# Optimization experiments

Measured on AMD Instinct MI355X. Metric: run time of the kernel, lower is better.

Reference implementation:

```python
import jax, jax.numpy as jnp
import numpy as np

EMBED_DIM = 2048
NUM_HEADS = 16
NUM_KV_GROUPS = 4
HEAD_DIM = EMBED_DIM // NUM_HEADS  # 128


def setup_inputs() -> dict:
    key = jax.random.key(0)
    ks = jax.random.split(key, 9)
    B, S, E = 2, 2048, EMBED_DIM
    kv_dim = HEAD_DIM * NUM_KV_GROUPS
    sc = 1.0 / np.sqrt(E)
    return {
        "x": jax.random.normal(ks[0], (B, S, E), dtype=jnp.float32),
        "Wq": jax.random.normal(ks[1], (E, E), dtype=jnp.float32) * sc,
        "bq": jnp.zeros((E,), dtype=jnp.float32),
        "Wk": jax.random.normal(ks[2], (E, kv_dim), dtype=jnp.float32) * sc,
        "bk": jnp.zeros((kv_dim,), dtype=jnp.float32),
        "Wv": jax.random.normal(ks[3], (E, kv_dim), dtype=jnp.float32) * sc,
        "bv": jnp.zeros((kv_dim,), dtype=jnp.float32),
        "Wo": jax.random.normal(ks[4], (E, E), dtype=jnp.float32) * sc,
        "bo": jnp.zeros((E,), dtype=jnp.float32),
    }


def reference(x, Wq, bq, Wk, bk, Wv, bv, Wo, bo):
    B, S, E = x.shape
    H, G, D = NUM_HEADS, NUM_KV_GROUPS, HEAD_DIM
    R = H // G  # heads per kv group
    # projections
    Q = (x @ Wq + bq).reshape(B, S, H, D).transpose(0, 2, 1, 3)   # [B,H,S,D]
    K = (x @ Wk + bk).reshape(B, S, G, D).transpose(0, 2, 1, 3)   # [B,G,S,D]
    V = (x @ Wv + bv).reshape(B, S, G, D).transpose(0, 2, 1, 3)   # [B,G,S,D]
    # GQA: broadcast KV groups over head subgroups instead of repeat_interleave copy
    Qg = Q.reshape(B, G, R, S, D)
    scores = jnp.einsum('bgrsd,bgtd->bgrst', Qg, K) / np.sqrt(D)  # [B,G,R,S,S]
    weights = jax.nn.softmax(scores, axis=-1)
    out = jnp.einsum('bgrst,bgtd->bgrsd', weights, V)             # [B,G,R,S,D]
    out = out.reshape(B, H, S, D).transpose(0, 2, 1, 3).reshape(B, S, E)
    return out @ Wo + bo
```

## Files before the change

kernel.cpp:

```cpp
#include <hip/hip_runtime.h>
#include <hip/hip_bf16.h>


typedef __attribute__((ext_vector_type(8))) short bf16x8;
typedef __attribute__((ext_vector_type(4))) short bf16x4;
typedef __attribute__((ext_vector_type(4))) float f32x4;

#define MFMA_16x16x32(a, b, c) __builtin_amdgcn_mfma_f32_16x16x32_bf16((a), (b), (c), 0, 0, 0)

__device__ __forceinline__ unsigned short f2bf(float x) {
  union { float f; unsigned int u; } c;
  c.f = x;
  unsigned int u = c.u;
  return (unsigned short)((u + 0x7fffu + ((u >> 16) & 1u)) >> 16);
}

__device__ __forceinline__ unsigned short f2bf_hw(float x) {
  __hip_bfloat16 h = __float2bfloat16(x);
  union { __hip_bfloat16 h; unsigned short u; } c;
  c.h = h;
  return c.u;
}

__device__ __forceinline__ void gload_lds16(const void* g, void* l) {
  __builtin_amdgcn_global_load_lds(
      (const __attribute__((address_space(1))) unsigned int*)g,
      (__attribute__((address_space(3))) unsigned int*)l, 16, 0, 0);
}

__global__ void cast_x_kernel(const float* __restrict__ x,
                              unsigned short* __restrict__ out, long n) {
  long i = ((long)blockIdx.x * blockDim.x + threadIdx.x) * 8;
  if (i >= n) return;
  float4 a = *reinterpret_cast<const float4*>(x + i);
  float4 b = *reinterpret_cast<const float4*>(x + i + 4);
  union { unsigned short s[8]; bf16x8 v; } o;
  o.s[0] = f2bf(a.x); o.s[1] = f2bf(a.y); o.s[2] = f2bf(a.z); o.s[3] = f2bf(a.w);
  o.s[4] = f2bf(b.x); o.s[5] = f2bf(b.y); o.s[6] = f2bf(b.z); o.s[7] = f2bf(b.w);
  *reinterpret_cast<bf16x8*>(out + i) = o.v;
}

__global__ void prep_w_kernel(const float* __restrict__ Wq,
                              const float* __restrict__ Wk,
                              const float* __restrict__ Wv,
                              const float* __restrict__ Wo,
                              unsigned short* __restrict__ WqkvT,
                              unsigned short* __restrict__ WoT) {
  __shared__ float t[32][33];
  const int tx = threadIdx.x, ty = threadIdx.y;
  const int ng = blockIdx.x * 32;
  const int k0 = blockIdx.y * 32;
  const float* src;
  int srcN, n0;
  unsigned short* dst;
  if (ng < 2048)      { src = Wq; srcN = 2048; n0 = ng;        dst = WqkvT + (size_t)ng * 2048; }
  else if (ng < 2560) { src = Wk; srcN = 512;  n0 = ng - 2048; dst = WqkvT + (size_t)ng * 2048; }
  else if (ng < 3072) { src = Wv; srcN = 512;  n0 = ng - 2560; dst = WqkvT + (size_t)ng * 2048; }
  else                { src = Wo; srcN = 2048; n0 = ng - 3072; dst = WoT + (size_t)(ng - 3072) * 2048; }
#pragma unroll
  for (int i = 0; i < 4; i++)
    t[ty + i * 8][tx] = src[(size_t)(k0 + ty + i * 8) * srcN + n0 + tx];
  __syncthreads();
#pragma unroll
  for (int i = 0; i < 4; i++)
    dst[(size_t)(ty + i * 8) * 2048 + k0 + tx] = f2bf(t[tx][ty + i * 8]);
}

__global__ void concat_bias_kernel(const float* __restrict__ bq,
                                   const float* __restrict__ bk,
                                   const float* __restrict__ bv,
                                   float* __restrict__ out) {
  int i = blockIdx.x * 256 + threadIdx.x;
  if (i >= 3072) return;
  out[i] = (i < 2048) ? bq[i] : (i < 2560 ? bk[i - 2048] : bv[i - 2560]);
}

template <int AROWS, int BROWS, bool BF16OUT>
__global__ __launch_bounds__(512, 2)
void gemm_pipe_kernel(const unsigned short* __restrict__ A,
                      const unsigned short* __restrict__ Bt,
                      const float* __restrict__ bias,
                      void* __restrict__ C, int M, int N, int K,
                      float qscale, int qcols,
                      unsigned short* __restrict__ vt) {
  constexpr int FM = AROWS / 32;
  constexpr int FN = BROWS / 64;
  constexpr int HFM = FM / 2;
  constexpr int TC = (AROWS + BROWS) * 4;
  constexpr int LOADS = (TC + 511) / 512;
  constexpr int PC = LOADS * 512;
  constexpr int BUFE = PC * 8;
  constexpr int BOFF = AROWS * 32;
  constexpr int LH = (LOADS + 1) / 2;
  __shared__ unsigned short lds[4 * BUFE];

  const int tid = threadIdx.x;
  const int w = tid >> 6, l = tid & 63, lg = l >> 4, ll = l & 15;
  const int wm = w >> 2, wn = w & 3;
  const int m0 = blockIdx.y * AROWS;
  const int n0 = blockIdx.x * BROWS;
  const int NT = K >> 5;

  const f32x4 fz = {0.f, 0.f, 0.f, 0.f};
  f32x4 acc[FM][FN];
#pragma unroll
  for (int i = 0; i < FM; i++)
#pragma unroll
    for (int j = 0; j < FN; j++) acc[i][j] = fz;

  const unsigned short* gsrc[LOADS];
#pragma unroll
  for (int i = 0; i < LOADS; ++i) {
    const int c = tid + 512 * i;
    if (c < AROWS * 4) {
      gsrc[i] = A + (size_t)(m0 + (c >> 2)) * K + (c & 3) * 8;
    } else if (c < TC) {
      const int cb = c - AROWS * 4;
      gsrc[i] = Bt + (size_t)(n0 + (cb >> 2)) * K + (cb & 3) * 8;
    } else {
      gsrc[i] = Bt + (size_t)n0 * K;
    }
  }

  auto stage_lo = [&](int t) {
    unsigned short* dst = &lds[(t & 3) * BUFE + tid * 8];
#pragma unroll
    for (int i = 0; i < LH; ++i) gload_lds16(gsrc[i] + t * 32, dst + i * 4096);
  };
  auto stage_hi = [&](int t) {
    unsigned short* dst = &lds[(t & 3) * BUFE + tid * 8];
#pragma unroll
    for (int i = LH; i < LOADS; ++i) gload_lds16(gsrc[i] + t * 32, dst + i * 4096);
  };

  stage_lo(0); stage_hi(0);
  stage_lo(1); stage_hi(1);

  for (int t = 0; t < NT; ++t) {
    if (t + 1 < NT) {
      if constexpr (LOADS == 4)
        asm volatile("s_waitcnt vmcnt(4)" ::: "memory");
      else if constexpr (LOADS == 3)
        asm volatile("s_waitcnt vmcnt(3)" ::: "memory");
      else
        asm volatile("s_waitcnt vmcnt(0)" ::: "memory");
    } else {
      asm volatile("s_waitcnt vmcnt(0)" ::: "memory");
    }
    __builtin_amdgcn_s_barrier();
    const unsigned short* bufp = &lds[(t & 3) * BUFE];

    bf16x8 bfrag[FN], afrag[HFM];
#pragma unroll
    for (int ni = 0; ni < FN; ++ni)
      bfrag[ni] = *reinterpret_cast<const bf16x8*>(
          &bufp[BOFF + (wn * FN * 16 + ni * 16 + ll) * 32 + lg * 8]);
#pragma unroll
    for (int mi = 0; mi < HFM; ++mi)
      afrag[mi] = *reinterpret_cast<const bf16x8*>(
          &bufp[(wm * (AROWS / 2) + mi * 16 + ll) * 32 + lg * 8]);
    if (t + 2 < NT) stage_lo(t + 2);
    __builtin_amdgcn_s_setprio(1);
#pragma unroll
    for (int mi = 0; mi < HFM; ++mi)
#pragma unroll
      for (int ni = 0; ni < FN; ++ni)
        acc[mi][ni] = MFMA_16x16x32(afrag[mi], bfrag[ni], acc[mi][ni]);
    __builtin_amdgcn_s_setprio(0);

#pragma unroll
    for (int mi = 0; mi < HFM; ++mi)
      afrag[mi] = *reinterpret_cast<const bf16x8*>(
          &bufp[(wm * (AROWS / 2) + (HFM + mi) * 16 + ll) * 32 + lg * 8]);
    if (t + 2 < NT) stage_hi(t + 2);
    __builtin_amdgcn_s_setprio(1);
#pragma unroll
    for (int mi = 0; mi < HFM; ++mi)
#pragma unroll
      for (int ni = 0; ni < FN; ++ni)
        acc[HFM + mi][ni] = MFMA_16x16x32(afrag[mi], bfrag[ni], acc[HFM + mi][ni]);
    __builtin_amdgcn_s_setprio(0);
  }

#pragma unroll
  for (int mi = 0; mi < FM; ++mi) {
#pragma unroll
    for (int ni = 0; ni < FN; ++ni) {
      const int gc = n0 + wn * FN * 16 + ni * 16 + ll;
      const float bv = bias[gc];
      const float sc = (gc < qcols) ? qscale : 1.0f;
      if (BF16OUT && vt != nullptr && gc >= 2560) {
        const int gr0 = m0 + wm * (AROWS / 2) + mi * 16 + 4 * lg;
        const int bb = gr0 >> 11, s = gr0 & 2047;
        const int spb = (s & ~63) | ((s & 12) << 1) | (((s >> 4) & 1) << 2) | (s & 32);
        union { unsigned short u[4]; bf16x4 v4; } ov;
#pragma unroll
        for (int r = 0; r < 4; ++r) ov.u[r] = f2bf(acc[mi][ni][r] + bv);
        *reinterpret_cast<bf16x4*>(
            &vt[(size_t)(bb * 512 + gc - 2560) * 2048 + spb]) = ov.v4;
      } else {
#pragma unroll
        for (int r = 0; r < 4; ++r) {
          const int gr = m0 + wm * (AROWS / 2) + mi * 16 + 4 * lg + r;
          const float v = (acc[mi][ni][r] + bv) * sc;
          if constexpr (BF16OUT)
            ((unsigned short*)C)[(size_t)gr * N + gc] = f2bf(v);
          else
            ((float*)C)[(size_t)gr * N + gc] = v;
        }
      }
    }
  }
}

__global__ __launch_bounds__(256, 2)
void attn_kernel(const unsigned short* __restrict__ QKV,
                 const unsigned short* __restrict__ Vt,
                 unsigned short* __restrict__ AO) {
  __shared__ unsigned short Klds[2][64 * 128];
  __shared__ unsigned short Vlds[2][128 * 64];

  const int tid = threadIdx.x;
  const int w = tid >> 6, l = tid & 63, lg = l >> 4, ll = l & 15;
  const int bh = blockIdx.y;
  const int b = bh >> 4, h = bh & 15, g = h >> 2;
  const int q0 = blockIdx.x * 128 + w * 32;
  const size_t row_base = (size_t)b * 2048 * 2560;
  const unsigned short* Vg = Vt + (size_t)(b * 512 + g * 128) * 2048;

  bf16x8 qf[2][4];
#pragma unroll
  for (int mi = 0; mi < 2; mi++)
#pragma unroll
    for (int ds = 0; ds < 4; ds++)
      qf[mi][ds] = *reinterpret_cast<const bf16x8*>(
          QKV + row_base + (size_t)(q0 + mi * 16 + ll) * 2560 + h * 128 + ds * 32 + 8 * lg);

  const f32x4 fz = {0.f, 0.f, 0.f, 0.f};
  f32x4 o[8][2];
#pragma unroll
  for (int di = 0; di < 8; di++)
#pragma unroll
    for (int mi = 0; mi < 2; mi++) o[di][mi] = fz;
  float pssum[2] = {0.f, 0.f};

  const int krow = tid >> 4, kc8 = tid & 15;
  const int vrow = tid >> 3, vc8 = tid & 7;
  const unsigned short* Kg = QKV + row_base + 2048 + g * 128 + kc8 * 8 + (size_t)krow * 2560;
  int klo[4], vlo[4];
#pragma unroll
  for (int i = 0; i < 4; i++) {
    const int kr = krow + 16 * i;
    klo[i] = (kr * 128 + kc8 * 8) ^ ((kr & 7) << 3);
    const int vr = vrow + 32 * i;
    vlo[i] = (vr * 64 + vc8 * 8) ^ ((vr & 7) << 3);
  }

  bf16x8 kreg[4], vreg[4];
#pragma unroll
  for (int i = 0; i < 4; i++) {
    kreg[i] = *reinterpret_cast<const bf16x8*>(Kg + (size_t)(16 * i) * 2560);
    vreg[i] = *reinterpret_cast<const bf16x8*>(Vg + (size_t)(vrow + 32 * i) * 2048 + vc8 * 8);
  }

  for (int kt = 0; kt < 32; kt++) {
    const int cb = kt & 1;
#pragma unroll
    for (int i = 0; i < 4; i++) *reinterpret_cast<bf16x8*>(&Klds[cb][klo[i]]) = kreg[i];
#pragma unroll
    for (int i = 0; i < 4; i++) *reinterpret_cast<bf16x8*>(&Vlds[cb][vlo[i]]) = vreg[i];
    __syncthreads();

    if (kt + 1 < 32) {
#pragma unroll
      for (int i = 0; i < 4; i++) {
        kreg[i] = *reinterpret_cast<const bf16x8*>(
            Kg + (size_t)((kt + 1) * 64 + 16 * i) * 2560);
        vreg[i] = *reinterpret_cast<const bf16x8*>(
            Vg + (size_t)(vrow + 32 * i) * 2048 + (kt + 1) * 64 + vc8 * 8);
      }
    }

    f32x4 st[4][2];
#pragma unroll
    for (int ni = 0; ni < 4; ni++)
#pragma unroll
      for (int mi = 0; mi < 2; mi++) st[ni][mi] = fz;
#pragma unroll
    for (int ds = 0; ds < 4; ds++) {
      bf16x8 kf[4];
#pragma unroll
      for (int ni = 0; ni < 4; ni++) {
        const int kr = ni * 16 + ll;
        kf[ni] = *reinterpret_cast<const bf16x8*>(
            &Klds[cb][(kr * 128 + ds * 32 + 8 * lg) ^ ((kr & 7) << 3)]);
      }
      __builtin_amdgcn_s_setprio(1);
#pragma unroll
      for (int ni = 0; ni < 4; ni++)
#pragma unroll
        for (int mi = 0; mi < 2; mi++)
          st[ni][mi] = MFMA_16x16x32(kf[ni], qf[mi][ds], st[ni][mi]);
      __builtin_amdgcn_s_setprio(0);
    }

#pragma unroll
    for (int ni = 0; ni < 4; ni++)
#pragma unroll
      for (int mi = 0; mi < 2; mi++)
#pragma unroll
        for (int r = 0; r < 4; r++) {
          const float pv = __builtin_amdgcn_exp2f(st[ni][mi][r]);
          st[ni][mi][r] = pv;
          pssum[mi] += pv;
        }

    bf16x8 pf[2][2];
#pragma unroll
    for (int mi = 0; mi < 2; mi++)
#pragma unroll
      for (int ks = 0; ks < 2; ks++)
#pragma unroll
        for (int j = 0; j < 4; j++) {
          pf[mi][ks][j]     = (short)f2bf_hw(st[2 * ks][mi][j]);
          pf[mi][ks][4 + j] = (short)f2bf_hw(st[2 * ks + 1][mi][j]);
        }

    __builtin_amdgcn_s_setprio(1);
#pragma unroll
    for (int ks = 0; ks < 2; ks++)
#pragma unroll
      for (int di = 0; di < 8; di++) {
        const int dr = di * 16 + ll;
        const bf16x8 vf = *reinterpret_cast<const bf16x8*>(
            &Vlds[cb][(dr * 64 + ks * 32 + 8 * lg) ^ ((dr & 7) << 3)]);
        o[di][0] = MFMA_16x16x32(vf, pf[0][ks], o[di][0]);
        o[di][1] = MFMA_16x16x32(vf, pf[1][ks], o[di][1]);
      }
    __builtin_amdgcn_s_setprio(0);
  }

  float invl[2];
#pragma unroll
  for (int mi = 0; mi < 2; mi++) {
    float s = pssum[mi];
    s += __shfl_xor(s, 16, 64);
    s += __shfl_xor(s, 32, 64);
    invl[mi] = 1.0f / s;
  }
#pragma unroll
  for (int mi = 0; mi < 2; mi++) {
    const size_t rowoff = (size_t)(b * 2048 + q0 + mi * 16 + ll) * 2048 + h * 128;
#pragma unroll
    for (int di = 0; di < 8; di++) {
      union { unsigned short s[4]; bf16x4 v; } ov;
#pragma unroll
      for (int r = 0; r < 4; r++) ov.s[r] = f2bf_hw(o[di][mi][r] * invl[mi]);
      *reinterpret_cast<bf16x4*>(&AO[rowoff + di * 16 + 4 * lg]) = ov.v;
    }
  }
}

extern "C" void kernel_launch(void* const* d_in, const int* in_sizes, int n_in,
                              void* d_out, int out_size, void* d_ws, size_t ws_size,
                              hipStream_t stream) {
  const float* x  = (const float*)d_in[0];
  const float* Wq = (const float*)d_in[1];
  const float* bq = (const float*)d_in[2];
  const float* Wk = (const float*)d_in[3];
  const float* bk = (const float*)d_in[4];
  const float* Wv = (const float*)d_in[5];
  const float* bv = (const float*)d_in[6];
  const float* Wo = (const float*)d_in[7];
  const float* bo = (const float*)d_in[8];
  float* out = (float*)d_out;

  unsigned short* xb    = (unsigned short*)d_ws;
  unsigned short* WqkvT = xb + (size_t)4096 * 2048;
  unsigned short* WoT   = WqkvT + (size_t)3072 * 2048;
  unsigned short* QKV   = WoT + (size_t)2048 * 2048;
  unsigned short* AO    = QKV + (size_t)4096 * 2560;
  unsigned short* Vt    = AO + (size_t)4096 * 2048;
  float* bqkv = (float*)(Vt + (size_t)1024 * 2048);

  const float QSC2 = 0.08838834764831845f * 1.4426950408889634f;

  cast_x_kernel<<<4096, 256, 0, stream>>>(x, xb, (long)8388608);
  prep_w_kernel<<<dim3(160, 64), dim3(32, 8), 0, stream>>>(Wq, Wk, Wv, Wo, WqkvT, WoT);
  concat_bias_kernel<<<12, 256, 0, stream>>>(bq, bk, bv, bqkv);

  gemm_pipe_kernel<256, 192, true><<<dim3(16, 16), 512, 0, stream>>>(
      xb, WqkvT, bqkv, QKV, 4096, 2560, 2048, QSC2, 2048, Vt);
  attn_kernel<<<dim3(16, 32), 256, 0, stream>>>(QKV, Vt, AO);
  gemm_pipe_kernel<128, 256, false><<<dim3(8, 32), 512, 0, stream>>>(
      AO, WoT, bo, out, 4096, 2048, 2048, 1.0f, 0, nullptr);
}
```

Measured before the change: 190.7 us.

## Split GEMM K-step into multi-phase ping-pong schedule with per-phase barriers

Restructures the GEMM main loop so each K-tile runs in 2 or 4 phases. Each phase loads an A-fragment slice, issues one slice of the global-to-LDS prefetch for tile t+2, then crosses a barrier before its MFMA block, and a second barrier ends the phase. The vmcnt wait moves to the end of the last phase. The aim is to interleave memory issue with MFMA more finely and keep waves in lockstep, in the style of a ping-pong schedule. In exchange it adds many more barriers per K-step, which could stall waves.

```diff
diff --git a/kernel.cpp b/kernel.cpp
--- a/kernel.cpp
+++ b/kernel.cpp
@@ -85,13 +85,13 @@
                       unsigned short* __restrict__ vt) {
   constexpr int FM = AROWS / 32;
   constexpr int FN = BROWS / 64;
-  constexpr int HFM = FM / 2;
   constexpr int TC = (AROWS + BROWS) * 4;
   constexpr int LOADS = (TC + 511) / 512;
   constexpr int PC = LOADS * 512;
   constexpr int BUFE = PC * 8;
   constexpr int BOFF = AROWS * 32;
-  constexpr int LH = (LOADS + 1) / 2;
+  constexpr int NPH = (FM >= 8) ? 4 : 2;
+  constexpr int RPP = FM / NPH;
   __shared__ unsigned short lds[4 * BUFE];
 
   const int tid = threadIdx.x;
@@ -122,64 +122,73 @@
     }
   }
 
-  auto stage_lo = [&](int t) {
-    unsigned short* dst = &lds[(t & 3) * BUFE + tid * 8];
-#pragma unroll
-    for (int i = 0; i < LH; ++i) gload_lds16(gsrc[i] + t * 32, dst + i * 4096);
-  };
-  auto stage_hi = [&](int t) {
-    unsigned short* dst = &lds[(t & 3) * BUFE + tid * 8];
-#pragma unroll
-    for (int i = LH; i < LOADS; ++i) gload_lds16(gsrc[i] + t * 32, dst + i * 4096);
-  };
-
-  stage_lo(0); stage_hi(0);
-  stage_lo(1); stage_hi(1);
+#pragma unroll
+  for (int g = 0; g < LOADS; ++g)
+    gload_lds16(gsrc[g], &lds[tid * 8 + g * 4096]);
+#pragma unroll
+  for (int g = 0; g < LOADS; ++g)
+    gload_lds16(gsrc[g] + 32, &lds[BUFE + tid * 8 + g * 4096]);
+  if constexpr (LOADS == 4)
+    asm volatile("s_waitcnt vmcnt(4)" ::: "memory");
+  else
+    asm volatile("s_waitcnt vmcnt(3)" ::: "memory");
+  __builtin_amdgcn_s_barrier();
 
   for (int t = 0; t < NT; ++t) {
-    if (t + 1 < NT) {
-      if constexpr (LOADS == 4)
-        asm volatile("s_waitcnt vmcnt(4)" ::: "memory");
-      else if constexpr (LOADS == 3)
-        asm volatile("s_waitcnt vmcnt(3)" ::: "memory");
-      else
-        asm volatile("s_waitcnt vmcnt(0)" ::: "memory");
-    } else {
-      asm volatile("s_waitcnt vmcnt(0)" ::: "memory");
-    }
-    __builtin_amdgcn_s_barrier();
     const unsigned short* bufp = &lds[(t & 3) * BUFE];
-
-    bf16x8 bfrag[FN], afrag[HFM];
-#pragma unroll
-    for (int ni = 0; ni < FN; ++ni)
-      bfrag[ni] = *reinterpret_cast<const bf16x8*>(
-          &bufp[BOFF + (wn * FN * 16 + ni * 16 + ll) * 32 + lg * 8]);
-#pragma unroll
-    for (int mi = 0; mi < HFM; ++mi)
-      afrag[mi] = *reinterpret_cast<const bf16x8*>(
-          &bufp[(wm * (AROWS / 2) + mi * 16 + ll) * 32 + lg * 8]);
-    if (t + 2 < NT) stage_lo(t + 2);
-    __builtin_amdgcn_s_setprio(1);
-#pragma unroll
-    for (int mi = 0; mi < HFM; ++mi)
-#pragma unroll
-      for (int ni = 0; ni < FN; ++ni)
-        acc[mi][ni] = MFMA_16x16x32(afrag[mi], bfrag[ni], acc[mi][ni]);
-    __builtin_amdgcn_s_setprio(0);
-
-#pragma unroll
-    for (int mi = 0; mi < HFM; ++mi)
-      afrag[mi] = *reinterpret_cast<const bf16x8*>(
-          &bufp[(wm * (AROWS / 2) + (HFM + mi) * 16 + ll) * 32 + lg * 8]);
-    if (t + 2 < NT) stage_hi(t + 2);
-    __builtin_amdgcn_s_setprio(1);
-#pragma unroll
-    for (int mi = 0; mi < HFM; ++mi)
-#pragma unroll
-      for (int ni = 0; ni < FN; ++ni)
-        acc[HFM + mi][ni] = MFMA_16x16x32(afrag[mi], bfrag[ni], acc[HFM + mi][ni]);
-    __builtin_amdgcn_s_setprio(0);
+    unsigned short* sdst = &lds[((t + 2) & 3) * BUFE + tid * 8];
+    const bool dostage = (t + 2 < NT);
+    bf16x8 bfrag[FN];
+#pragma unroll
+    for (int p = 0; p < NPH; ++p) {
+      if (p == 0) {
+#pragma unroll
+        for (int ni = 0; ni < FN; ++ni)
+          bfrag[ni] = *reinterpret_cast<const bf16x8*>(
+              &bufp[BOFF + (wn * FN * 16 + ni * 16 + ll) * 32 + lg * 8]);
+      }
+      bf16x8 afrag[RPP];
+#pragma unroll
+      for (int r = 0; r < RPP; ++r)
+        afrag[r] = *reinterpret_cast<const bf16x8*>(
+            &bufp[(wm * (AROWS / 2) + (p * RPP + r) * 16 + ll) * 32 + lg * 8]);
+      if (dostage) {
+        if constexpr (NPH == 4) {
+          if (p < LOADS)
+            gload_lds16(gsrc[p] + (t + 2) * 32, sdst + p * 4096);
+        } else {
+          if (p == 0) {
+            gload_lds16(gsrc[0] + (t + 2) * 32, sdst);
+            gload_lds16(gsrc[1] + (t + 2) * 32, sdst + 4096);
+          } else {
+#pragma unroll
+            for (int g = 2; g < LOADS; ++g)
+              gload_lds16(gsrc[g] + (t + 2) * 32, sdst + g * 4096);
+          }
+        }
+      }
+      __builtin_amdgcn_s_barrier();
+      asm volatile("s_waitcnt lgkmcnt(0)" ::: "memory");
+      __builtin_amdgcn_s_setprio(1);
+#pragma unroll
+      for (int r = 0; r < RPP; ++r)
+#pragma unroll
+        for (int ni = 0; ni < FN; ++ni)
+          acc[p * RPP + r][ni] =
+              MFMA_16x16x32(afrag[r], bfrag[ni], acc[p * RPP + r][ni]);
+      __builtin_amdgcn_s_setprio(0);
+      if (p == NPH - 1 && t + 1 < NT) {
+        if (dostage) {
+          if constexpr (LOADS == 4)
+            asm volatile("s_waitcnt vmcnt(4)" ::: "memory");
+          else
+            asm volatile("s_waitcnt vmcnt(3)" ::: "memory");
+        } else {
+          asm volatile("s_waitcnt vmcnt(0)" ::: "memory");
+        }
+      }
+      __builtin_amdgcn_s_barrier();
+    }
   }
 
 #pragma unroll
```

Result: slower. 200.7 us (+5.2%).
